# Performance work log

Measured on AMD Instinct MI355X. Metric: run time of the kernel, lower is better.

The kernel has to match this reference:

```python
import jax, jax.numpy as jnp
import numpy as np

EPS = 1e-12  # F.normalize default eps (norm clamped to at least eps)


def setup_inputs() -> dict:
    key = jax.random.key(0)
    k1, k2, k3, k4 = jax.random.split(key, 4)
    B, Cin, Cout, H, W = 8, 128, 32, 256, 256
    x = jax.random.normal(k1, (B, Cin, H, W), dtype=jnp.float32)
    qk = jax.random.normal(k2, (B, 2 * Cout, H, W), dtype=jnp.float32)
    # 1x1 conv params (PyTorch Conv2d default init scale ~ 1/sqrt(fan_in))
    w_v = jax.random.normal(k3, (Cout, Cin), dtype=jnp.float32) / np.sqrt(Cin)
    b_v = jax.random.normal(k4, (Cout,), dtype=jnp.float32) / np.sqrt(Cin)
    temperature = jnp.ones((1, 1, 1), dtype=jnp.float32)
    return {"x": x, "qk": qk, "w_v": w_v, "b_v": b_v, "temperature": temperature}


def reference(x, qk, w_v, b_v, temperature):
    B, Cin, H, W = x.shape
    Co = w_v.shape[0]
    N = H * W
    # 1x1 conv == channel GEMM
    v = jnp.einsum('bchw,oc->bohw', x, w_v) + b_v[None, :, None, None]
    # split qk: k = first Co channels, q = last Co channels; head=1
    q = qk[:, Co:].reshape(B, 1, Co, N)
    k = qk[:, :Co].reshape(B, 1, Co, N)
    v = v.reshape(B, 1, Co, N)
    # L2-normalize over spatial dim (F.normalize: divide by max(norm, eps))
    q = q / jnp.maximum(jnp.linalg.norm(q, axis=-1, keepdims=True), EPS)
    k = k / jnp.maximum(jnp.linalg.norm(k, axis=-1, keepdims=True), EPS)
    # channel-wise (transposed) attention: [B,1,Co,Co]
    attn = jnp.einsum('bhcn,bhdn->bhcd', q, k) * temperature
    attn = jax.nn.softmax(attn, axis=-1)
    out = jnp.einsum('bhcd,bhdn->bhcn', attn, v)  # [B,1,Co,N]
    return out
```

## Files before the change

kernel.cpp:

```cpp
#include <hip/hip_runtime.h>
#include <hip/hip_bf16.h>
#include <math.h>

#define NB    8
#define CIN   128
#define CO    32
#define CH    64
#define NN    65536
#define CPB   512
#define GBLK  (NN/CPB)
#define TCOLS 128
#define NTILES (CPB/TCOLS)

typedef __attribute__((ext_vector_type(8))) short bf16x8;
typedef __attribute__((ext_vector_type(16))) float f32x16;

__device__ __forceinline__ short f2bf(float f) {
    union { __hip_bfloat16 h; short s; } u;
    u.h = __float2bfloat16(f);
    return u.s;
}
__device__ __forceinline__ float bf2f(short s) {
    union { __hip_bfloat16 h; short s; } u;
    u.s = s;
    return __bfloat162float(u.h);
}

__global__ __launch_bounds__(256) void gram_kernel(const float* __restrict__ qk,
                                                   float* __restrict__ part,
                                                   float* __restrict__ partsq) {
    __shared__ float smem[CH * TCOLS];
    float4* tile4 = (float4*)smem;

    const int b = blockIdx.y;
    const int blk = blockIdx.x;
    const int t = threadIdx.x;
    const int w = t >> 6;
    const int l = t & 63;
    const int c = l & 31;
    const int half = l >> 5;

    const float* qkb = qk + (size_t)b * CH * NN;
    const size_t colbase0 = (size_t)blk * CPB;

    const int lrow[8] = {  (t) >> 5, (t + 256) >> 5, (t + 512) >> 5, (t + 768) >> 5,
                           (t + 1024) >> 5, (t + 1280) >> 5, (t + 1536) >> 5, (t + 1792) >> 5 };
    const int lcol4 = t & 31;

    f32x16 acc = {};
    float sq[8] = {0.f, 0.f, 0.f, 0.f, 0.f, 0.f, 0.f, 0.f};

    float4 st[8];
#pragma unroll
    for (int k = 0; k < 8; ++k)
        st[k] = *(const float4*)(qkb + (size_t)lrow[k] * NN + colbase0 + lcol4 * 4);

#pragma unroll
    for (int tau = 0; tau < NTILES; ++tau) {
#pragma unroll
        for (int k = 0; k < 8; ++k) {
            float4 v = st[k];
            sq[k] = fmaf(v.x, v.x, sq[k]);
            sq[k] = fmaf(v.y, v.y, sq[k]);
            sq[k] = fmaf(v.z, v.z, sq[k]);
            sq[k] = fmaf(v.w, v.w, sq[k]);
            tile4[lrow[k] * 32 + (lcol4 ^ (lrow[k] & 7))] = v;
        }
        __syncthreads();

        if (tau + 1 < NTILES) {
            const size_t colbase = colbase0 + (size_t)(tau + 1) * TCOLS;
#pragma unroll
            for (int k = 0; k < 8; ++k)
                st[k] = *(const float4*)(qkb + (size_t)lrow[k] * NN + colbase + lcol4 * 4);
        }

#pragma unroll
        for (int ss = 0; ss < 2; ++ss) {
            const int s = 2 * w + ss;
            const int f0 = s * 4 + half * 2;
            const int qrow = CO + c;
            const int krow = c;
            const int sw = c & 7;
            float4 q0 = tile4[qrow * 32 + (f0 ^ sw)];
            float4 q1 = tile4[qrow * 32 + ((f0 + 1) ^ sw)];
            float4 k0 = tile4[krow * 32 + (f0 ^ sw)];
            float4 k1 = tile4[krow * 32 + ((f0 + 1) ^ sw)];

            float qf[8] = {q0.x, q0.y, q0.z, q0.w, q1.x, q1.y, q1.z, q1.w};
            float kf[8] = {k0.x, k0.y, k0.z, k0.w, k1.x, k1.y, k1.z, k1.w};

            bf16x8 ah, al, bh, bl;
#pragma unroll
            for (int j = 0; j < 8; ++j) {
                short hq = f2bf(qf[j]);
                ah[j] = hq;
                al[j] = f2bf(qf[j] - bf2f(hq));
                short hk = f2bf(kf[j]);
                bh[j] = hk;
                bl[j] = f2bf(kf[j] - bf2f(hk));
            }
            acc = __builtin_amdgcn_mfma_f32_32x32x16_bf16(ah, bh, acc, 0, 0, 0);
            acc = __builtin_amdgcn_mfma_f32_32x32x16_bf16(ah, bl, acc, 0, 0, 0);
            acc = __builtin_amdgcn_mfma_f32_32x32x16_bf16(al, bh, acc, 0, 0, 0);
        }
        __syncthreads();
    }

#pragma unroll
    for (int r = 0; r < 16; ++r) {
        int row = (r & 3) + 8 * (r >> 2) + 4 * half;
        smem[w * 1024 + row * 32 + c] = acc[r];
    }
#pragma unroll
    for (int k = 0; k < 8; ++k)
        smem[4096 + ((t >> 5) + 8 * k) * 32 + (t & 31)] = sq[k];
    __syncthreads();

    float* pp = part + ((size_t)b * GBLK + blk) * 1024;
#pragma unroll
    for (int j = 0; j < 4; ++j) {
        int idx = t + j * 256;
        pp[idx] = smem[idx] + smem[1024 + idx] + smem[2048 + idx] + smem[3072 + idx];
    }
    if (t < 64) {
        float s = 0.f;
#pragma unroll
        for (int i = 0; i < 32; ++i) s += smem[4096 + t * 32 + i];
        partsq[((size_t)b * GBLK + blk) * 64 + t] = s;
    }
}

__global__ __launch_bounds__(128) void reduce_kernel(const float* __restrict__ part,
                                                     const float* __restrict__ partsq,
                                                     float* __restrict__ Sred) {
    const int b = blockIdx.y;
    const int v = blockIdx.x * 64 + (threadIdx.x >> 1);
    const int h = threadIdx.x & 1;
    float s = 0.f;
    if (v < 1024) {
        const float* p = part + (size_t)b * GBLK * 1024 + v;
        for (int ch = h * (GBLK / 2); ch < (h + 1) * (GBLK / 2); ++ch)
            s += p[(size_t)ch * 1024];
    } else {
        const float* p = partsq + (size_t)b * GBLK * 64 + (v - 1024);
        for (int ch = h * (GBLK / 2); ch < (h + 1) * (GBLK / 2); ++ch)
            s += p[(size_t)ch * 64];
    }
    s += __shfl_xor(s, 1);
    if (h == 0) Sred[b * 1088 + v] = s;
}

__global__ __launch_bounds__(256) void attn_kernel(const float* __restrict__ Sred,
                                                   const float* __restrict__ w_v,
                                                   const float* __restrict__ b_v,
                                                   const float* __restrict__ temp,
                                                   unsigned short* __restrict__ Whi,
                                                   unsigned short* __restrict__ Wlo,
                                                   float* __restrict__ beff) {
    __shared__ float sS[1024];
    __shared__ float snorm[64];
    __shared__ float sA[1024];
    const int t = threadIdx.x;
    const int b = blockIdx.x;

    for (int i = t; i < 1024; i += 256) sS[i] = Sred[b * 1088 + i];
    if (t < 64) snorm[t] = fmaxf(sqrtf(Sred[b * 1088 + 1024 + t]), 1e-12f);
    __syncthreads();

    if (t < 32) {
        const float T = temp[0];
        const float qn = snorm[32 + t];
        float m = -1e30f;
        for (int d = 0; d < 32; ++d)
            m = fmaxf(m, sS[t * 32 + d] / (qn * snorm[d]) * T);
        float sum = 0.f;
        for (int d = 0; d < 32; ++d)
            sum += expf(sS[t * 32 + d] / (qn * snorm[d]) * T - m);
        const float inv = 1.f / sum;
        for (int d = 0; d < 32; ++d)
            sA[t * 32 + d] = expf(sS[t * 32 + d] / (qn * snorm[d]) * T - m) * inv;
    }
    __syncthreads();

    for (int idx = t; idx < CO * CIN; idx += 256) {
        int cc = idx >> 7;
        int ci = idx & 127;
        float s = 0.f;
#pragma unroll
        for (int d = 0; d < 32; ++d) s += sA[cc * 32 + d] * w_v[d * CIN + ci];
        short hi = f2bf(s);
        short lo = f2bf(s - bf2f(hi));
        Whi[(size_t)b * CO * CIN + idx] = (unsigned short)hi;
        Wlo[(size_t)b * CO * CIN + idx] = (unsigned short)lo;
    }
    if (t < 32) {
        float s = 0.f;
#pragma unroll
        for (int d = 0; d < 32; ++d) s += sA[t * 32 + d] * b_v[d];
        beff[b * CO + t] = s;
    }
}

__global__ __launch_bounds__(256) void out_kernel(const float* __restrict__ x,
                                                  const unsigned short* __restrict__ Whi,
                                                  const unsigned short* __restrict__ Wlo,
                                                  const float* __restrict__ beff,
                                                  float* __restrict__ out) {
    const int b = blockIdx.y;
    const int t = threadIdx.x;
    const int w = t >> 6;
    const int l = t & 63;
    const int c = l & 31;
    const int half = l >> 5;

    const float* xb = x + (size_t)b * CIN * NN;

    bf16x8 ah[8], al[8];
    {
        const unsigned short* Wh = Whi + (size_t)b * CO * CIN + c * CIN + half * 8;
        const unsigned short* Wl = Wlo + (size_t)b * CO * CIN + c * CIN + half * 8;
#pragma unroll
        for (int s = 0; s < 8; ++s) {
            ah[s] = *(const bf16x8*)(Wh + s * 16);
            al[s] = *(const bf16x8*)(Wl + s * 16);
        }
    }
    float bias[16];
    {
        const float* bb = beff + b * CO;
#pragma unroll
        for (int r = 0; r < 16; ++r)
            bias[r] = bb[(r & 3) + 8 * (r >> 2) + 4 * half];
    }

#pragma unroll
    for (int tile = 0; tile < 4; ++tile) {
        const int col = blockIdx.x * 512 + w * 128 + tile * 32 + c;
        f32x16 acc = {};
#pragma unroll
        for (int s = 0; s < 8; ++s) {
            const float* xp = xb + (size_t)(s * 16 + half * 8) * NN + col;
            float xv[8];
#pragma unroll
            for (int j = 0; j < 8; ++j) xv[j] = xp[(size_t)j * NN];
            bf16x8 bh, bl;
#pragma unroll
            for (int j = 0; j < 8; ++j) {
                short h = f2bf(xv[j]);
                bh[j] = h;
                bl[j] = f2bf(xv[j] - bf2f(h));
            }
            acc = __builtin_amdgcn_mfma_f32_32x32x16_bf16(ah[s], bh, acc, 0, 0, 0);
            acc = __builtin_amdgcn_mfma_f32_32x32x16_bf16(ah[s], bl, acc, 0, 0, 0);
            acc = __builtin_amdgcn_mfma_f32_32x32x16_bf16(al[s], bh, acc, 0, 0, 0);
        }
        float* ob = out + (size_t)b * CO * NN + col;
#pragma unroll
        for (int r = 0; r < 16; ++r) {
            int o = (r & 3) + 8 * (r >> 2) + 4 * half;
            ob[(size_t)o * NN] = acc[r] + bias[r];
        }
    }
}

extern "C" void kernel_launch(void* const* d_in, const int* in_sizes, int n_in,
                              void* d_out, int out_size, void* d_ws, size_t ws_size,
                              hipStream_t stream) {
    const float* x    = (const float*)d_in[0];
    const float* qk   = (const float*)d_in[1];
    const float* w_v  = (const float*)d_in[2];
    const float* b_v  = (const float*)d_in[3];
    const float* temp = (const float*)d_in[4];
    float* out = (float*)d_out;

    float* part   = (float*)d_ws;
    float* partsq = part + (size_t)NB * GBLK * 1024;
    float* Sred   = partsq + (size_t)NB * GBLK * 64;
    unsigned short* Whi = (unsigned short*)(Sred + (size_t)NB * 1088);
    unsigned short* Wlo = Whi + (size_t)NB * CO * CIN;
    float* beff   = (float*)(Wlo + (size_t)NB * CO * CIN);

    gram_kernel<<<dim3(GBLK, NB), 256, 0, stream>>>(qk, part, partsq);
    reduce_kernel<<<dim3(17, NB), 128, 0, stream>>>(part, partsq, Sred);
    attn_kernel<<<dim3(NB), 256, 0, stream>>>(Sred, w_v, b_v, temp, Whi, Wlo, beff);
    out_kernel<<<dim3(NN / 512, NB), 256, 0, stream>>>(x, Whi, Wlo, beff, out);
}
```

Measured before the change: 121.1 us.

## Stage x tile in swizzled LDS with float4 loads, one tile per block

```diff
diff --git a/kernel.cpp b/kernel.cpp
--- a/kernel.cpp
+++ b/kernel.cpp
@@ -207,6 +207,9 @@
                                                   const unsigned short* __restrict__ Wlo,
                                                   const float* __restrict__ beff,
                                                   float* __restrict__ out) {
+    __shared__ float4 tile4[CIN * 32];
+    const float* lf = (const float*)tile4;
+
     const int b = blockIdx.y;
     const int t = threadIdx.x;
     const int w = t >> 6;
@@ -215,6 +218,7 @@
     const int half = l >> 5;
 
     const float* xb = x + (size_t)b * CIN * NN;
+    const int col0 = blockIdx.x * 128;
 
     bf16x8 ah[8], al[8];
     {
@@ -226,41 +230,52 @@
             al[s] = *(const bf16x8*)(Wl + s * 16);
         }
     }
-    float bias[16];
-    {
-        const float* bb = beff + b * CO;
-#pragma unroll
-        for (int r = 0; r < 16; ++r)
-            bias[r] = bb[(r & 3) + 8 * (r >> 2) + 4 * half];
-    }
-
-#pragma unroll
-    for (int tile = 0; tile < 4; ++tile) {
-        const int col = blockIdx.x * 512 + w * 128 + tile * 32 + c;
-        f32x16 acc = {};
-#pragma unroll
-        for (int s = 0; s < 8; ++s) {
-            const float* xp = xb + (size_t)(s * 16 + half * 8) * NN + col;
-            float xv[8];
-#pragma unroll
-            for (int j = 0; j < 8; ++j) xv[j] = xp[(size_t)j * NN];
-            bf16x8 bh, bl;
-#pragma unroll
-            for (int j = 0; j < 8; ++j) {
-                short h = f2bf(xv[j]);
-                bh[j] = h;
-                bl[j] = f2bf(xv[j] - bf2f(h));
-            }
-            acc = __builtin_amdgcn_mfma_f32_32x32x16_bf16(ah[s], bh, acc, 0, 0, 0);
-            acc = __builtin_amdgcn_mfma_f32_32x32x16_bf16(ah[s], bl, acc, 0, 0, 0);
-            acc = __builtin_amdgcn_mfma_f32_32x32x16_bf16(al[s], bh, acc, 0, 0, 0);
-        }
-        float* ob = out + (size_t)b * CO * NN + col;
-#pragma unroll
-        for (int r = 0; r < 16; ++r) {
-            int o = (r & 3) + 8 * (r >> 2) + 4 * half;
-            ob[(size_t)o * NN] = acc[r] + bias[r];
-        }
+
+    float4 st[16];
+#pragma unroll
+    for (int k = 0; k < 16; ++k) {
+        int flat = t + k * 256;
+        int ci = flat >> 5;
+        int col4 = flat & 31;
+        st[k] = *(const float4*)(xb + (size_t)ci * NN + col0 + col4 * 4);
+    }
+#pragma unroll
+    for (int k = 0; k < 16; ++k) {
+        int flat = t + k * 256;
+        int ci = flat >> 5;
+        int col4 = flat & 31;
+        tile4[ci * 32 + (col4 ^ (ci & 7))] = st[k];
+    }
+    __syncthreads();
+
+    const int n = w * 32 + c;
+    f32x16 acc = {};
+#pragma unroll
+    for (int s = 0; s < 8; ++s) {
+        float xv[8];
+#pragma unroll
+        for (int j = 0; j < 8; ++j) {
+            int ci = s * 16 + half * 8 + j;
+            xv[j] = lf[(ci * 32 + ((n >> 2) ^ (ci & 7))) * 4 + (n & 3)];
+        }
+        bf16x8 bh, bl;
+#pragma unroll
+        for (int j = 0; j < 8; ++j) {
+            short h = f2bf(xv[j]);
+            bh[j] = h;
+            bl[j] = f2bf(xv[j] - bf2f(h));
+        }
+        acc = __builtin_amdgcn_mfma_f32_32x32x16_bf16(ah[s], bh, acc, 0, 0, 0);
+        acc = __builtin_amdgcn_mfma_f32_32x32x16_bf16(ah[s], bl, acc, 0, 0, 0);
+        acc = __builtin_amdgcn_mfma_f32_32x32x16_bf16(al[s], bh, acc, 0, 0, 0);
+    }
+
+    const float* bb = beff + b * CO;
+    float* ob = out + (size_t)b * CO * NN + col0 + n;
+#pragma unroll
+    for (int r = 0; r < 16; ++r) {
+        int o = (r & 3) + 8 * (r >> 2) + 4 * half;
+        ob[(size_t)o * NN] = acc[r] + bb[o];
     }
 }
 
@@ -284,5 +299,5 @@
     gram_kernel<<<dim3(GBLK, NB), 256, 0, stream>>>(qk, part, partsq);
     reduce_kernel<<<dim3(17, NB), 128, 0, stream>>>(part, partsq, Sred);
     attn_kernel<<<dim3(NB), 256, 0, stream>>>(Sred, w_v, b_v, temp, Whi, Wlo, beff);
-    out_kernel<<<dim3(NN / 512, NB), 256, 0, stream>>>(x, Whi, Wlo, beff, out);
-}
+    out_kernel<<<dim3(NN / 128, NB), 256, 0, stream>>>(x, Whi, Wlo, beff, out);
+}
```

Result: slower. 127.4 us (+5.2%).

## Stage x tiles through swizzled LDS with float4 loads and register prefetch

Applied to the files above, without the earlier changes.

```diff
diff --git a/kernel.cpp b/kernel.cpp
--- a/kernel.cpp
+++ b/kernel.cpp
@@ -207,6 +207,9 @@
                                                   const unsigned short* __restrict__ Wlo,
                                                   const float* __restrict__ beff,
                                                   float* __restrict__ out) {
+    __shared__ float4 tile4[CIN * 32];
+    const float* lf = (const float*)tile4;
+
     const int b = blockIdx.y;
     const int t = threadIdx.x;
     const int w = t >> 6;
@@ -215,6 +218,7 @@
     const int half = l >> 5;
 
     const float* xb = x + (size_t)b * CIN * NN;
+    const int col0 = blockIdx.x * 512;
 
     bf16x8 ah[8], al[8];
     {
@@ -234,16 +238,45 @@
             bias[r] = bb[(r & 3) + 8 * (r >> 2) + 4 * half];
     }
 
-#pragma unroll
-    for (int tile = 0; tile < 4; ++tile) {
-        const int col = blockIdx.x * 512 + w * 128 + tile * 32 + c;
+    const int lci   = t >> 5;
+    const int lcol4 = t & 31;
+
+    float4 st[16];
+#pragma unroll
+    for (int k = 0; k < 16; ++k) {
+        int ci = lci + k * 8;
+        st[k] = *(const float4*)(xb + (size_t)ci * NN + col0 + lcol4 * 4);
+    }
+
+    const int n = w * 32 + c;
+
+#pragma unroll
+    for (int tau = 0; tau < 4; ++tau) {
+#pragma unroll
+        for (int k = 0; k < 16; ++k) {
+            int ci = lci + k * 8;
+            tile4[ci * 32 + (lcol4 ^ (ci & 7))] = st[k];
+        }
+        __syncthreads();
+
+        if (tau < 3) {
+            const int colb = col0 + (tau + 1) * 128;
+#pragma unroll
+            for (int k = 0; k < 16; ++k) {
+                int ci = lci + k * 8;
+                st[k] = *(const float4*)(xb + (size_t)ci * NN + colb + lcol4 * 4);
+            }
+        }
+
         f32x16 acc = {};
 #pragma unroll
         for (int s = 0; s < 8; ++s) {
-            const float* xp = xb + (size_t)(s * 16 + half * 8) * NN + col;
             float xv[8];
 #pragma unroll
-            for (int j = 0; j < 8; ++j) xv[j] = xp[(size_t)j * NN];
+            for (int j = 0; j < 8; ++j) {
+                int ci = s * 16 + half * 8 + j;
+                xv[j] = lf[(ci * 32 + ((n >> 2) ^ (ci & 7))) * 4 + (n & 3)];
+            }
             bf16x8 bh, bl;
 #pragma unroll
             for (int j = 0; j < 8; ++j) {
@@ -255,12 +288,14 @@
             acc = __builtin_amdgcn_mfma_f32_32x32x16_bf16(ah[s], bl, acc, 0, 0, 0);
             acc = __builtin_amdgcn_mfma_f32_32x32x16_bf16(al[s], bh, acc, 0, 0, 0);
         }
-        float* ob = out + (size_t)b * CO * NN + col;
+
+        float* ob = out + (size_t)b * CO * NN + col0 + tau * 128 + n;
 #pragma unroll
         for (int r = 0; r < 16; ++r) {
             int o = (r & 3) + 8 * (r >> 2) + 4 * half;
             ob[(size_t)o * NN] = acc[r] + bias[r];
         }
+        __syncthreads();
     }
 }
 
```

Result: slower. 182.8 us (+50.9%).
